# Optimization experiments

Measured on AMD Instinct MI355X. Metric: run time of the kernel, lower is better.

Reference implementation:

```python
import jax, jax.numpy as jnp
import numpy as np

B, S, HID = 2, 2048, 2048
NH, HD = 16, 128            # num heads, head dim (HID = NH*HD)
ROT = 64                    # rotary_dim
MASK_VALUE = -10000.0


def _rotate_every_two(x):
    # x: [..., d] with d even; interleaved (-x2, x1)
    x1 = x[..., ::2]
    x2 = x[..., 1::2]
    return jnp.stack((-x2, x1), axis=-1).reshape(x.shape)


def _fixed_sincos(seq_len, dim):
    inv_freq = 1.0 / (10000.0 ** (jnp.arange(0, dim, 2, dtype=jnp.float32) / dim))
    t = jnp.arange(seq_len, dtype=jnp.float32)
    ang = t[:, None] * inv_freq[None, :]          # [S, dim/2]
    return jnp.sin(ang), jnp.cos(ang)


def _apply_rope(x, sin, cos):
    # x: [B, S, H, rot]; sin/cos: [S, rot/2] -> repeat_interleave(2) -> [S, rot]
    sin = jnp.repeat(sin, 2, axis=-1)[None, :, None, :]
    cos = jnp.repeat(cos, 2, axis=-1)[None, :, None, :]
    return x * cos + _rotate_every_two(x) * sin


def setup_inputs() -> dict:
    key = jax.random.key(0)
    ks = jax.random.split(key, 7)
    w_scale = 1.0 / np.sqrt(HID)
    return {
        "hidden_states": jax.random.normal(ks[0], (B, S, HID), dtype=jnp.float32),
        "attention_mask": jnp.zeros((B, 1, 1, S), dtype=jnp.float32),
        "Wq": jax.random.normal(ks[1], (HID, HID), dtype=jnp.float32) * w_scale,
        "bq": jnp.zeros((HID,), dtype=jnp.float32),
        "Wk": jax.random.normal(ks[2], (HID, HID), dtype=jnp.float32) * w_scale,
        "bk": jnp.zeros((HID,), dtype=jnp.float32),
        "Wv": jax.random.normal(ks[3], (HID, HID), dtype=jnp.float32) * w_scale,
        "bv": jnp.zeros((HID,), dtype=jnp.float32),
    }


def reference(hidden_states, attention_mask, Wq, bq, Wk, bk, Wv, bv):
    # QKV projections (torch Linear: x @ W.T + b)
    q = (hidden_states @ Wq.T + bq).reshape(B, S, NH, HD)
    k = (hidden_states @ Wk.T + bk).reshape(B, S, NH, HD)
    v = (hidden_states @ Wv.T + bv).reshape(B, S, NH, HD)

    # Inline rotary on first ROT dims of q/k
    sin, cos = _fixed_sincos(S, ROT)
    q = jnp.concatenate([_apply_rope(q[..., :ROT], sin, cos), q[..., ROT:]], axis=-1)
    k = jnp.concatenate([_apply_rope(k[..., :ROT], sin, cos), k[..., ROT:]], axis=-1)

    # Scores [B, H, S, S]
    scores = jnp.einsum('bqhd,bkhd->bhqk', q, k) / np.sqrt(HD)

    # Causal mask + additive attention mask
    causal = jnp.tril(jnp.ones((S, S), dtype=bool))[None, None]
    scores = jnp.where(causal, scores, jnp.asarray(MASK_VALUE, scores.dtype))
    scores = scores + attention_mask

    probs = jax.nn.softmax(scores, axis=-1)
    ctx = jnp.einsum('bhqk,bkhd->bqhd', probs, v)
    return ctx.reshape(B, S, HID)
```

## Files before the change

### kernel.cpp

```cpp
#include <hip/hip_runtime.h>

typedef unsigned short bhalf;
typedef __attribute__((ext_vector_type(4))) float    f32x4;
typedef __attribute__((ext_vector_type(8))) short    s16x8;
typedef __attribute__((ext_vector_type(4))) float    floatx4;
typedef __attribute__((ext_vector_type(4))) unsigned int u32x4;
typedef __attribute__((ext_vector_type(4))) unsigned short u16x4;

#define B_  2
#define S_  2048
#define HID_ 2048
#define NH_ 16
#define HD_ 128
#define M_  (B_*S_)
#define MASKV (-10000.0f)

__device__ __forceinline__ bhalf f32_to_bf16(float f) {
    union { float f; unsigned int u; } v; v.f = f;
    unsigned int r = v.u + 0x7FFFu + ((v.u >> 16) & 1u);
    return (bhalf)(r >> 16);
}
__device__ __forceinline__ bhalf f32_to_bf16_trunc(float f) {
    union { float f; unsigned int u; } v; v.f = f;
    return (bhalf)(v.u >> 16);
}
__device__ __forceinline__ float bf16_to_f32(bhalf h) {
    union { unsigned int u; float f; } v; v.u = ((unsigned int)h) << 16;
    return v.f;
}

__device__ __forceinline__ void gl_lds16(const void* g, void* l) {
    __builtin_amdgcn_global_load_lds(
        (const __attribute__((address_space(1))) void*)g,
        (__attribute__((address_space(3))) void*)l, 16, 0, 0);
}

__global__ __launch_bounds__(256) void cast_all(const float* __restrict__ hs,
                                                const float* __restrict__ Wq,
                                                const float* __restrict__ Wk,
                                                const float* __restrict__ Wv,
                                                bhalf* __restrict__ dst) {
    int idx = blockIdx.x * 256 + threadIdx.x;
    const float* src;
    if (idx < 2097152)      src = hs + (size_t)idx * 4;
    else if (idx < 3145728) src = Wq + (size_t)(idx - 2097152) * 4;
    else if (idx < 4194304) src = Wk + (size_t)(idx - 3145728) * 4;
    else                    src = Wv + (size_t)(idx - 4194304) * 4;
    floatx4 f = *(const floatx4*)src;
    u16x4 o;
    o.x = f32_to_bf16(f.x); o.y = f32_to_bf16(f.y);
    o.z = f32_to_bf16(f.z); o.w = f32_to_bf16(f.w);
    *(u16x4*)(dst + (size_t)idx * 4) = o;
}

__global__ __launch_bounds__(256) void qkv_gemm(const bhalf* __restrict__ A,
                                                const bhalf* __restrict__ Wb,
                                                const float* __restrict__ bq,
                                                const float* __restrict__ bk,
                                                const float* __restrict__ bv,
                                                bhalf* __restrict__ Out,
                                                bhalf* __restrict__ VTo) {
    __shared__ __align__(16) bhalf As[128 * 32];
    __shared__ __align__(16) bhalf Bs[128 * 32];
    const int tid  = threadIdx.x;
    const int lane = tid & 63, w = tid >> 6;
    const int wy = w >> 1, wx = w & 1;
    const int quad = lane >> 4, l = lane & 15;
    const int m0 = blockIdx.x * 128, n0 = blockIdx.y * 128;
    const int z  = blockIdx.z;
    const bhalf* W    = Wb + (size_t)z * HID_ * HID_;
    const float* bias = (z == 0) ? bq : (z == 1) ? bk : bv;
    bhalf* out        = Out + (size_t)z * M_ * HID_;

    f32x4 acc[4][4] = {};

    for (int kt = 0; kt < HID_; kt += 32) {
#pragma unroll
        for (int j = 0; j < 2; ++j) {
            int slot0 = j * 256 + w * 64;
            int slot  = slot0 + lane;
            int row = slot >> 2;
            int cg  = (slot & 3) ^ ((row >> 1) & 3);
            gl_lds16(A + (size_t)(m0 + row) * HID_ + kt + cg * 8, As + slot0 * 8);
            gl_lds16(W + (size_t)(n0 + row) * HID_ + kt + cg * 8, Bs + slot0 * 8);
        }
        __syncthreads();
        s16x8 af[4], bfr[4];
#pragma unroll
        for (int mt = 0; mt < 4; ++mt) {
            int row = wy * 64 + mt * 16 + l;
            int cgs = quad ^ ((row >> 1) & 3);
            af[mt] = *(const s16x8*)(As + (row * 4 + cgs) * 8);
        }
#pragma unroll
        for (int nt = 0; nt < 4; ++nt) {
            int row = wx * 64 + nt * 16 + l;
            int cgs = quad ^ ((row >> 1) & 3);
            bfr[nt] = *(const s16x8*)(Bs + (row * 4 + cgs) * 8);
        }
#pragma unroll
        for (int mt = 0; mt < 4; ++mt)
#pragma unroll
            for (int nt = 0; nt < 4; ++nt)
                acc[mt][nt] = __builtin_amdgcn_mfma_f32_16x16x32_bf16(
                    af[mt], bfr[nt], acc[mt][nt], 0, 0, 0);
        __syncthreads();
    }
    if (z == 2) {
#pragma unroll
        for (int mt = 0; mt < 4; ++mt) {
#pragma unroll
            for (int nt = 0; nt < 4; ++nt) {
                int col = n0 + wx * 64 + nt * 16 + l;
                float bv_ = bias[col];
                int row0 = m0 + wy * 64 + mt * 16 + quad * 4;
                int bb = row0 >> 11, s0 = row0 & 2047;
                u16x4 o;
#pragma unroll
                for (int r = 0; r < 4; ++r) o[r] = f32_to_bf16(acc[mt][nt][r] + bv_);
                *(u16x4*)(VTo + ((size_t)(bb * 16) * 128 + col) * S_ + s0) = o;
            }
        }
    } else {
#pragma unroll
        for (int mt = 0; mt < 4; ++mt) {
#pragma unroll
            for (int nt = 0; nt < 4; ++nt) {
                int col = n0 + wx * 64 + nt * 16 + l;
                float bv_ = bias[col];
#pragma unroll
                for (int r = 0; r < 4; ++r) {
                    int row = m0 + wy * 64 + mt * 16 + quad * 4 + r;
                    out[(size_t)row * HID_ + col] = f32_to_bf16(acc[mt][nt][r] + bv_);
                }
            }
        }
    }
}

__global__ __launch_bounds__(256) void rope_table(float2* __restrict__ tab) {
    int idx = blockIdx.x * 256 + threadIdx.x;
    int i = idx & 31, s = idx >> 5;
    float inv = expf(-(float)i * 0.2878231366242557f);
    float ang = (float)s * inv;
    tab[idx] = make_float2(sinf(ang), cosf(ang));
}

__global__ __launch_bounds__(256) void rope_apply(bhalf* __restrict__ Qb,
                                                  bhalf* __restrict__ Kb,
                                                  const float2* __restrict__ tab) {
    int flat = blockIdx.x * 256 + threadIdx.x;
    int i = flat & 31;
    int h = (flat >> 5) & 15;
    int s = (flat >> 9) & 2047;
    int b = flat >> 20;
    size_t base = ((size_t)(b * S_ + s)) * HID_ + h * HD_ + 2 * i;
    float2 sc = tab[s * 32 + i];
    float c = sc.y, sn = sc.x;
    {
        unsigned int q = *(const unsigned int*)(Qb + base);
        float x0 = bf16_to_f32((bhalf)(q & 0xffff));
        float x1 = bf16_to_f32((bhalf)(q >> 16));
        unsigned int o = (unsigned int)f32_to_bf16(x0 * c - x1 * sn)
                       | ((unsigned int)f32_to_bf16(x1 * c + x0 * sn) << 16);
        *(unsigned int*)(Qb + base) = o;
    }
    {
        unsigned int k = *(const unsigned int*)(Kb + base);
        float x0 = bf16_to_f32((bhalf)(k & 0xffff));
        float x1 = bf16_to_f32((bhalf)(k >> 16));
        unsigned int o = (unsigned int)f32_to_bf16(x0 * c - x1 * sn)
                       | ((unsigned int)f32_to_bf16(x1 * c + x0 * sn) << 16);
        *(unsigned int*)(Kb + base) = o;
    }
}

__global__ __launch_bounds__(512, 2) void flash_attn(const bhalf* __restrict__ Qb,
                                                     const bhalf* __restrict__ Kb,
                                                     const bhalf* __restrict__ VT,
                                                     const float* __restrict__ amask,
                                                     float* __restrict__ out) {
    __shared__ __align__(16) bhalf Kbuf[2][2048 * 8];
    __shared__ __align__(16) bhalf Vbuf[2][2048 * 8];
    const int tid = threadIdx.x, lane = tid & 63, w = tid >> 6;
    const int quad = lane >> 4, l = lane & 15;
    const int qt = blockIdx.x, bh = blockIdx.y;
    const int b = bh >> 4, h = bh & 15;
    const bool is_hi = (w < 4);
    const int ws = w & 3;
    const int myrow = is_hi ? ((31 - qt) * 64 + ws * 16) : (qt * 64 + ws * 16);
    const int ch_hi   = (33 - qt) >> 1;
    const int lo_last = (qt * 64 + 63) >> 7;
    const int my_last = is_hi ? (ch_hi - 1) : lo_last;

    s16x8 qf[4];
    {
        const bhalf* Qrow = Qb + (size_t)(b * S_ + myrow + l) * HID_ + h * HD_;
#pragma unroll
        for (int ks = 0; ks < 4; ++ks)
            qf[ks] = *(const s16x8*)(Qrow + ks * 32 + quad * 8);
    }
    s16x8 ones;
#pragma unroll
    for (int j = 0; j < 8; ++j) ones[j] = (short)0x3F80;

    float m_run[4] = {-1e30f, -1e30f, -1e30f, -1e30f};
    f32x4 l_acc = {};
    f32x4 acc[8] = {};
    const int fpl = ((l >> 2) << 1) | (l & 1);

#pragma unroll
    for (int j = 0; j < 4; ++j) {
        int slot0 = j * 512 + w * 64;
        int slot  = slot0 + lane;
        int row = slot >> 4, x = slot & 15;
        int g   = (x & 8) | ((x ^ row) & 7);
        gl_lds16(Kb + (size_t)(b * S_ + row) * HID_ + h * HD_ + g * 8,
                 &Kbuf[0][slot0 * 8]);
        gl_lds16(VT + ((size_t)bh * HD_ + row) * S_ + g * 8,
                 &Vbuf[0][slot0 * 8]);
    }

    for (int kc = 0; kc < ch_hi; ++kc) {
        const int cur = kc & 1, nxt = cur ^ 1;
        const int key0 = kc * 128;
        __syncthreads();

        const bool active = (kc <= my_last);
        const bool diag   = (kc == my_last);

        float am[8];
        if (active) {
#pragma unroll
            for (int nt = 0; nt < 8; ++nt) am[nt] = amask[b * S_ + key0 + nt * 16 + l];
        }
        if (kc + 1 < ch_hi) {
            const int key1 = key0 + 128;
#pragma unroll
            for (int j = 0; j < 4; ++j) {
                int slot0 = j * 512 + w * 64;
                int slot  = slot0 + lane;
                int row = slot >> 4, x = slot & 15;
                int g   = (x & 8) | ((x ^ row) & 7);
                gl_lds16(Kb + (size_t)(b * S_ + key1 + row) * HID_ + h * HD_ + g * 8,
                         &Kbuf[nxt][slot0 * 8]);
                gl_lds16(VT + ((size_t)bh * HD_ + row) * S_ + key1 + g * 8,
                         &Vbuf[nxt][slot0 * 8]);
            }
        }

        const bhalf* Kc = &Kbuf[cur][0];
        const bhalf* Vc = &Vbuf[cur][0];
        bhalf* Pw = &Kbuf[cur][0] + w * 2048;

        f32x4 s[8] = {};
        if (active) {
#pragma unroll
            for (int nt = 0; nt < 8; ++nt) {
                int key = nt * 16 + l;
#pragma unroll
                for (int ks = 0; ks < 4; ++ks) {
                    int dg = ks * 4 + quad;
                    int x  = (dg & 8) | ((dg ^ key) & 7);
                    s16x8 kf = *(const s16x8*)(Kc + (key * 16 + x) * 8);
                    s[nt] = __builtin_amdgcn_mfma_f32_16x16x32_bf16(qf[ks], kf, s[nt], 0, 0, 0);
                }
            }
        }
        __asm__ __volatile__("s_waitcnt lgkmcnt(0)\n\ts_barrier" ::: "memory");

        if (active) {
#pragma unroll
            for (int r = 0; r < 4; ++r) {
                const int qrow = myrow + quad * 4 + r;
                float p[8];
#pragma unroll
                for (int nt = 0; nt < 8; ++nt) {
                    float v = s[nt][r] * 0.08838834764831845f;
                    if (diag) { int key = key0 + nt * 16 + l; v = (key > qrow) ? MASKV : v; }
                    p[nt] = v + am[nt];
                }
                float mx = fmaxf(fmaxf(fmaxf(p[0], p[1]), fmaxf(p[2], p[3])),
                                 fmaxf(fmaxf(p[4], p[5]), fmaxf(p[6], p[7])));
#pragma unroll
                for (int msk = 1; msk < 16; msk <<= 1) mx = fmaxf(mx, __shfl_xor(mx, msk, 64));
                float m_new = fmaxf(m_run[r], mx);
                float alpha = __expf(m_run[r] - m_new);
                m_run[r] = m_new;
                const int m  = quad * 4 + r;
                const int fm = (quad << 1) | (r & 1);
#pragma unroll
                for (int nt = 0; nt < 8; ++nt) {
                    float e = __expf(p[nt] - m_new);
                    int key = nt * 16 + l;
                    Pw[(m * 16 + ((key >> 3) ^ fm)) * 8 + (key & 7)] = f32_to_bf16_trunc(e);
                }
                l_acc[r] *= alpha;
#pragma unroll
                for (int nt = 0; nt < 8; ++nt) acc[nt][r] *= alpha;
            }
#pragma unroll
            for (int kstep = 0; kstep < 4; ++kstep) {
                int kg = kstep * 4 + quad;
                s16x8 pf = *(const s16x8*)(Pw + (l * 16 + (kg ^ fpl)) * 8);
                l_acc = __builtin_amdgcn_mfma_f32_16x16x32_bf16(pf, ones, l_acc, 0, 0, 0);
#pragma unroll
                for (int nt = 0; nt < 8; ++nt) {
                    int d = nt * 16 + l;
                    int x = (kg & 8) | ((kg ^ d) & 7);
                    s16x8 vf = *(const s16x8*)(Vc + (d * 16 + x) * 8);
                    acc[nt] = __builtin_amdgcn_mfma_f32_16x16x32_bf16(pf, vf, acc[nt], 0, 0, 0);
                }
            }
        }
    }

    float inv[4];
#pragma unroll
    for (int r = 0; r < 4; ++r) inv[r] = 1.f / l_acc[r];
#pragma unroll
    for (int nt = 0; nt < 8; ++nt) {
        int col = h * HD_ + nt * 16 + l;
#pragma unroll
        for (int r = 0; r < 4; ++r)
            out[(size_t)(b * S_ + myrow + quad * 4 + r) * HID_ + col] = acc[nt][r] * inv[r];
    }
}

extern "C" void kernel_launch(void* const* d_in, const int* in_sizes, int n_in,
                              void* d_out, int out_size, void* d_ws, size_t ws_size,
                              hipStream_t stream) {
    const float* hs    = (const float*)d_in[0];
    const float* amask = (const float*)d_in[1];
    const float* Wq    = (const float*)d_in[2];
    const float* bq    = (const float*)d_in[3];
    const float* Wk    = (const float*)d_in[4];
    const float* bk    = (const float*)d_in[5];
    const float* Wv    = (const float*)d_in[6];
    const float* bv    = (const float*)d_in[7];
    float* out = (float*)d_out;

    bhalf* hsb = (bhalf*)d_ws;
    bhalf* wqb = hsb + 8388608;
    bhalf* wkb = wqb + 4194304;
    bhalf* wvb = wkb + 4194304;
    bhalf* Qb  = wvb + 4194304;
    bhalf* Kb  = Qb + 8388608;
    bhalf* VTb = Kb + 8388608;
    float2* tab = (float2*)(VTb + 8388608);

    rope_table<<<256, 256, 0, stream>>>(tab);
    cast_all<<<20480, 256, 0, stream>>>(hs, Wq, Wk, Wv, hsb);
    qkv_gemm<<<dim3(32, 16, 3), 256, 0, stream>>>(hsb, wqb, bq, bk, bv, Qb, VTb);
    rope_apply<<<8192, 256, 0, stream>>>(Qb, Kb, tab);
    flash_attn<<<dim3(16, 32), 512, 0, stream>>>(Qb, Kb, VTb, amask, out);
}
```

Before: 373.7 us.

## Fuse RoPE into QKV GEMM epilogue and widen GEMM K-tile to 64

Removes the separate rope_apply kernel. Rotary embedding is now applied in the Q/K GEMM epilogue, using a lane shuffle to fetch the paired element. This avoids a read-modify-write pass over Q and K in global memory and one kernel launch. It also doubles the GEMM K tile from 32 to 64 with an 8-way XOR swizzle, halving the number of barriers per K loop at the cost of double the LDS footprint per block.

```diff
diff --git a/kernel.cpp b/kernel.cpp
--- a/kernel.cpp
+++ b/kernel.cpp
@@ -4,7 +4,6 @@
 typedef __attribute__((ext_vector_type(4))) float    f32x4;
 typedef __attribute__((ext_vector_type(8))) short    s16x8;
 typedef __attribute__((ext_vector_type(4))) float    floatx4;
-typedef __attribute__((ext_vector_type(4))) unsigned int u32x4;
 typedef __attribute__((ext_vector_type(4))) unsigned short u16x4;
 
 #define B_  2
@@ -23,10 +22,6 @@
 __device__ __forceinline__ bhalf f32_to_bf16_trunc(float f) {
     union { float f; unsigned int u; } v; v.f = f;
     return (bhalf)(v.u >> 16);
-}
-__device__ __forceinline__ float bf16_to_f32(bhalf h) {
-    union { unsigned int u; float f; } v; v.u = ((unsigned int)h) << 16;
-    return v.f;
 }
 
 __device__ __forceinline__ void gl_lds16(const void* g, void* l) {
@@ -53,15 +48,24 @@
     *(u16x4*)(dst + (size_t)idx * 4) = o;
 }
 
+__global__ __launch_bounds__(256) void rope_table(float2* __restrict__ tab) {
+    int idx = blockIdx.x * 256 + threadIdx.x;
+    int i = idx & 31, s = idx >> 5;
+    float inv = expf(-(float)i * 0.2878231366242557f);
+    float ang = (float)s * inv;
+    tab[idx] = make_float2(sinf(ang), cosf(ang));
+}
+
 __global__ __launch_bounds__(256) void qkv_gemm(const bhalf* __restrict__ A,
                                                 const bhalf* __restrict__ Wb,
                                                 const float* __restrict__ bq,
                                                 const float* __restrict__ bk,
                                                 const float* __restrict__ bv,
+                                                const float2* __restrict__ tab,
                                                 bhalf* __restrict__ Out,
                                                 bhalf* __restrict__ VTo) {
-    __shared__ __align__(16) bhalf As[128 * 32];
-    __shared__ __align__(16) bhalf Bs[128 * 32];
+    __shared__ __align__(16) bhalf As[128 * 64];
+    __shared__ __align__(16) bhalf Bs[128 * 64];
     const int tid  = threadIdx.x;
     const int lane = tid & 63, w = tid >> 6;
     const int wy = w >> 1, wx = w & 1;
@@ -74,36 +78,44 @@
 
     f32x4 acc[4][4] = {};
 
-    for (int kt = 0; kt < HID_; kt += 32) {
-#pragma unroll
-        for (int j = 0; j < 2; ++j) {
+    for (int kt = 0; kt < HID_; kt += 64) {
+#pragma unroll
+        for (int j = 0; j < 4; ++j) {
             int slot0 = j * 256 + w * 64;
             int slot  = slot0 + lane;
-            int row = slot >> 2;
-            int cg  = (slot & 3) ^ ((row >> 1) & 3);
+            int row = slot >> 3;
+            int cg  = (slot & 7) ^ (row & 7);
             gl_lds16(A + (size_t)(m0 + row) * HID_ + kt + cg * 8, As + slot0 * 8);
             gl_lds16(W + (size_t)(n0 + row) * HID_ + kt + cg * 8, Bs + slot0 * 8);
         }
         __syncthreads();
-        s16x8 af[4], bfr[4];
+        s16x8 af[4][2], bfr[4][2];
 #pragma unroll
         for (int mt = 0; mt < 4; ++mt) {
             int row = wy * 64 + mt * 16 + l;
-            int cgs = quad ^ ((row >> 1) & 3);
-            af[mt] = *(const s16x8*)(As + (row * 4 + cgs) * 8);
+#pragma unroll
+            for (int ks = 0; ks < 2; ++ks) {
+                int kk = ks * 4 + quad;
+                af[mt][ks] = *(const s16x8*)(As + (row * 8 + (kk ^ (row & 7))) * 8);
+            }
         }
 #pragma unroll
         for (int nt = 0; nt < 4; ++nt) {
             int row = wx * 64 + nt * 16 + l;
-            int cgs = quad ^ ((row >> 1) & 3);
-            bfr[nt] = *(const s16x8*)(Bs + (row * 4 + cgs) * 8);
-        }
-#pragma unroll
-        for (int mt = 0; mt < 4; ++mt)
-#pragma unroll
-            for (int nt = 0; nt < 4; ++nt)
-                acc[mt][nt] = __builtin_amdgcn_mfma_f32_16x16x32_bf16(
-                    af[mt], bfr[nt], acc[mt][nt], 0, 0, 0);
+#pragma unroll
+            for (int ks = 0; ks < 2; ++ks) {
+                int kk = ks * 4 + quad;
+                bfr[nt][ks] = *(const s16x8*)(Bs + (row * 8 + (kk ^ (row & 7))) * 8);
+            }
+        }
+#pragma unroll
+        for (int ks = 0; ks < 2; ++ks)
+#pragma unroll
+            for (int mt = 0; mt < 4; ++mt)
+#pragma unroll
+                for (int nt = 0; nt < 4; ++nt)
+                    acc[mt][nt] = __builtin_amdgcn_mfma_f32_16x16x32_bf16(
+                        af[mt][ks], bfr[nt][ks], acc[mt][nt], 0, 0, 0);
         __syncthreads();
     }
     if (z == 2) {
@@ -121,12 +133,32 @@
                 *(u16x4*)(VTo + ((size_t)(bb * 16) * 128 + col) * S_ + s0) = o;
             }
         }
+    } else if (wx == 0) {
+#pragma unroll
+        for (int mt = 0; mt < 4; ++mt) {
+#pragma unroll
+            for (int nt = 0; nt < 4; ++nt) {
+                int col = n0 + nt * 16 + l;
+                float bv_ = bias[col];
+                int i = (nt * 16 + l) >> 1;
+#pragma unroll
+                for (int r = 0; r < 4; ++r) {
+                    int row = m0 + wy * 64 + mt * 16 + quad * 4 + r;
+                    float v  = acc[mt][nt][r] + bv_;
+                    float vp = __shfl_xor(v, 1, 64);
+                    float2 sc = tab[(row & 2047) * 32 + i];
+                    float y = (l & 1) ? (v * sc.y + vp * sc.x)
+                                      : (v * sc.y - vp * sc.x);
+                    out[(size_t)row * HID_ + col] = f32_to_bf16(y);
+                }
+            }
+        }
     } else {
 #pragma unroll
         for (int mt = 0; mt < 4; ++mt) {
 #pragma unroll
             for (int nt = 0; nt < 4; ++nt) {
-                int col = n0 + wx * 64 + nt * 16 + l;
+                int col = n0 + 64 + nt * 16 + l;
                 float bv_ = bias[col];
 #pragma unroll
                 for (int r = 0; r < 4; ++r) {
@@ -135,43 +167,6 @@
                 }
             }
         }
-    }
-}
-
-__global__ __launch_bounds__(256) void rope_table(float2* __restrict__ tab) {
-    int idx = blockIdx.x * 256 + threadIdx.x;
-    int i = idx & 31, s = idx >> 5;
-    float inv = expf(-(float)i * 0.2878231366242557f);
-    float ang = (float)s * inv;
-    tab[idx] = make_float2(sinf(ang), cosf(ang));
-}
-
-__global__ __launch_bounds__(256) void rope_apply(bhalf* __restrict__ Qb,
-                                                  bhalf* __restrict__ Kb,
-                                                  const float2* __restrict__ tab) {
-    int flat = blockIdx.x * 256 + threadIdx.x;
-    int i = flat & 31;
-    int h = (flat >> 5) & 15;
-    int s = (flat >> 9) & 2047;
-    int b = flat >> 20;
-    size_t base = ((size_t)(b * S_ + s)) * HID_ + h * HD_ + 2 * i;
-    float2 sc = tab[s * 32 + i];
-    float c = sc.y, sn = sc.x;
-    {
-        unsigned int q = *(const unsigned int*)(Qb + base);
-        float x0 = bf16_to_f32((bhalf)(q & 0xffff));
-        float x1 = bf16_to_f32((bhalf)(q >> 16));
-        unsigned int o = (unsigned int)f32_to_bf16(x0 * c - x1 * sn)
-                       | ((unsigned int)f32_to_bf16(x1 * c + x0 * sn) << 16);
-        *(unsigned int*)(Qb + base) = o;
-    }
-    {
-        unsigned int k = *(const unsigned int*)(Kb + base);
-        float x0 = bf16_to_f32((bhalf)(k & 0xffff));
-        float x1 = bf16_to_f32((bhalf)(k >> 16));
-        unsigned int o = (unsigned int)f32_to_bf16(x0 * c - x1 * sn)
-                       | ((unsigned int)f32_to_bf16(x1 * c + x0 * sn) << 16);
-        *(unsigned int*)(Kb + base) = o;
     }
 }
 
@@ -342,16 +337,13 @@
 
     bhalf* hsb = (bhalf*)d_ws;
     bhalf* wqb = hsb + 8388608;
-    bhalf* wkb = wqb + 4194304;
-    bhalf* wvb = wkb + 4194304;
-    bhalf* Qb  = wvb + 4194304;
+    bhalf* Qb  = wqb + 3 * 4194304;
     bhalf* Kb  = Qb + 8388608;
     bhalf* VTb = Kb + 8388608;
     float2* tab = (float2*)(VTb + 8388608);
 
     rope_table<<<256, 256, 0, stream>>>(tab);
     cast_all<<<20480, 256, 0, stream>>>(hs, Wq, Wk, Wv, hsb);
-    qkv_gemm<<<dim3(32, 16, 3), 256, 0, stream>>>(hsb, wqb, bq, bk, bv, Qb, VTb);
-    rope_apply<<<8192, 256, 0, stream>>>(Qb, Kb, tab);
+    qkv_gemm<<<dim3(32, 16, 3), 256, 0, stream>>>(hsb, wqb, bq, bk, bv, tab, Qb, VTb);
     flash_attn<<<dim3(16, 32), 512, 0, stream>>>(Qb, Kb, VTb, amask, out);
 }
```

Measured after the change: 462.0 us. 23.6% more time.
